# Kernel optimization log

Hardware: AMD Instinct MI355X
Metric: run time of the kernel (lower is better)

Reference implementation:

```python
import jax
jax.config.update("jax_enable_x64", True)
import jax.numpy as jnp
import numpy as np

N_VALUES = 33_554_432   # flattened JaggedTensor values (e.g. 16K batch x 2K multi-hot)
ZCH_SIZE = 4_194_304    # number of managed-collision slots
ID_MAX = 2_147_483_647  # input_hash_size - 1


def setup_inputs() -> dict:
    key = jax.random.key(0)
    k1, k2, k3 = jax.random.split(key, 3)
    values = jax.random.randint(k1, (N_VALUES,), 0, ID_MAX, dtype=jnp.int64)
    mch_sorted_raw_ids = jnp.sort(
        jax.random.randint(k2, (ZCH_SIZE,), 0, ID_MAX, dtype=jnp.int64)
    )
    # remapped ids are a permutation of [0, zch_size)
    mch_remapped_ids_mapping = jax.random.permutation(
        k3, jnp.arange(ZCH_SIZE, dtype=jnp.int64)
    )
    return {
        "values": values,
        "mch_sorted_raw_ids": mch_sorted_raw_ids,
        "mch_remapped_ids_mapping": mch_remapped_ids_mapping,
        "zch_index": ZCH_SIZE,
    }


def reference(values, mch_sorted_raw_ids, mch_remapped_ids_mapping, zch_index):
    # torch.searchsorted default (right=False) == jnp side='left'.
    # Search over table[:-1] so gathered index is always in-bounds (matches torch code).
    searched_indices = jnp.searchsorted(
        mch_sorted_raw_ids[:-1], values, side="left"
    )
    retrieved = mch_sorted_raw_ids[searched_indices]          # gather [N]
    remapped = mch_remapped_ids_mapping[searched_indices]     # gather [N]
    # fused masked-scatter equivalent: hit -> remapped id, miss -> zch sentinel
    return jnp.where(retrieved == values, remapped, jnp.int64(zch_index))
```

## Files before the change

kernel.cpp:

```cpp
#include <hip/hip_runtime.h>


typedef int vint4 __attribute__((ext_vector_type(4)));
typedef unsigned long long u64;

#define HK 2654435761u

__device__ __forceinline__ u64 sig_mask(unsigned v) {
    unsigned h = v * HK;
    return (1ULL << (h >> 26)) | (1ULL << ((h >> 20) & 63)) |
           (1ULL << ((h >> 14) & 63)) | (1ULL << ((h >> 8) & 63));
}

template <int BITS>
__global__ __launch_bounds__(256) void build_aux_scatter(
    const int* __restrict__ table, int m, int* __restrict__ aux) {
    const int SH = 31 - BITS;
    const unsigned NB = 1u << BITS;
    int j = blockIdx.x * blockDim.x + threadIdx.x;
    if (j >= m) return;
    unsigned lo_k = (j == 0) ? 0u : ((((unsigned)table[j - 1]) >> SH) + 1u);
    unsigned hi_k = ((unsigned)table[j]) >> SH;
    for (unsigned k = lo_k; k <= hi_k; ++k) aux[k] = j;
    if (j == m - 1) {
        for (unsigned k = hi_k + 1; k <= NB; ++k) aux[k] = m;
    }
}

template <int BITS>
__global__ __launch_bounds__(256) void build_sigs(
    const int* __restrict__ table, const int* __restrict__ aux, int z,
    u64* __restrict__ filter) {
    const int SH = 31 - BITS;
    const unsigned NB = 1u << BITS;
    unsigned k = blockIdx.x * blockDim.x + threadIdx.x;
    if (k >= NB) return;
    int p = aux[k];
    u64 sig = 0;
    while (p < z && ((((unsigned)table[p]) >> SH) == k)) {
        sig |= sig_mask((unsigned)table[p]);
        ++p;
    }
    filter[k] = sig;
}

template <int BITS>
__device__ __forceinline__ int resolve_window(
    int v, const int* __restrict__ table, const int* __restrict__ mapping,
    const int* __restrict__ aux, int z, int zch) {
    const int SH = 31 - BITS;
    unsigned k = ((unsigned)v) >> SH;
    int lo = aux[k];
    int hi = aux[k + 1];
    int s = lo & ~3;
    int e = (hi + 3) & ~3;
    if (e > z) e = z;
    int cnt = 0;
    bool eq = false;
    for (int p = s; p < e; p += 4) {
        int4 t = *(const int4*)(table + p);
        cnt += (t.x < v) + (t.y < v) + (t.z < v) + (t.w < v);
        eq = eq | (t.x == v) | (t.y == v) | (t.z == v) | (t.w == v);
    }
    if (eq) return mapping[s + cnt];
    return zch;
}

template <int BITS>
__global__ __launch_bounds__(256, 5) void mch_remap_bloom_kernel(
    const vint4* __restrict__ values4,
    const int* __restrict__ table,
    const int* __restrict__ mapping,
    const int* __restrict__ zch_p,
    const int* __restrict__ aux,
    const u64* __restrict__ filter,
    vint4* __restrict__ out4,
    int q4, int z) {
    const int SH = 31 - BITS;

    int zch = *zch_p;
    int i = blockIdx.x * blockDim.x + threadIdx.x;
    if (i >= q4) return;

    vint4 va = __builtin_nontemporal_load(values4 + i);
    vint4 vb = __builtin_nontemporal_load(values4 + i + q4);
    vint4 vc = __builtin_nontemporal_load(values4 + i + 2 * q4);
    vint4 vd = __builtin_nontemporal_load(values4 + i + 3 * q4);
    int v[16] = {va.x, va.y, va.z, va.w, vb.x, vb.y, vb.z, vb.w,
                 vc.x, vc.y, vc.z, vc.w, vd.x, vd.y, vd.z, vd.w};

    u64 w[16];
#pragma unroll
    for (int e = 0; e < 16; ++e) w[e] = filter[((unsigned)v[e]) >> SH];

    unsigned pm = 0;
#pragma unroll
    for (int e = 0; e < 16; ++e) {
        u64 mask = sig_mask((unsigned)v[e]);
        if ((w[e] & mask) == mask) pm |= (1u << e);
    }

    int r[16];
#pragma unroll
    for (int e = 0; e < 16; ++e) r[e] = zch;

    while (pm) {
        int e = __builtin_ctz(pm);
        pm &= pm - 1;
        int a0 = (e & 1) ? v[1]  : v[0];
        int a1 = (e & 1) ? v[3]  : v[2];
        int a2 = (e & 1) ? v[5]  : v[4];
        int a3 = (e & 1) ? v[7]  : v[6];
        int a4 = (e & 1) ? v[9]  : v[8];
        int a5 = (e & 1) ? v[11] : v[10];
        int a6 = (e & 1) ? v[13] : v[12];
        int a7 = (e & 1) ? v[15] : v[14];
        int b0 = (e & 2) ? a1 : a0;
        int b1 = (e & 2) ? a3 : a2;
        int b2 = (e & 2) ? a5 : a4;
        int b3 = (e & 2) ? a7 : a6;
        int c0 = (e & 4) ? b1 : b0;
        int c1 = (e & 4) ? b3 : b2;
        int ve = (e & 8) ? c1 : c0;

        int rr = resolve_window<BITS>(ve, table, mapping, aux, z, zch);

#pragma unroll
        for (int j = 0; j < 16; ++j) r[j] = (e == j) ? rr : r[j];
    }

    vint4 oa, ob, oc, od;
    oa.x = r[0];  oa.y = r[1];  oa.z = r[2];  oa.w = r[3];
    ob.x = r[4];  ob.y = r[5];  ob.z = r[6];  ob.w = r[7];
    oc.x = r[8];  oc.y = r[9];  oc.z = r[10]; oc.w = r[11];
    od.x = r[12]; od.y = r[13]; od.z = r[14]; od.w = r[15];
    __builtin_nontemporal_store(oa, out4 + i);
    __builtin_nontemporal_store(ob, out4 + i + q4);
    __builtin_nontemporal_store(oc, out4 + i + 2 * q4);
    __builtin_nontemporal_store(od, out4 + i + 3 * q4);
}

template <int BITS>
__global__ __launch_bounds__(64) void mch_remap_tail_kernel(
    const int* __restrict__ values, const int* __restrict__ table,
    const int* __restrict__ mapping, const int* __restrict__ zch_p,
    const int* __restrict__ aux, const u64* __restrict__ filter,
    int* __restrict__ out, int start, int n, int z) {
    const int SH = 31 - BITS;
    int i = start + blockIdx.x * blockDim.x + threadIdx.x;
    if (i >= n) return;
    int v = values[i];
    u64 w = filter[((unsigned)v) >> SH];
    u64 mask = sig_mask((unsigned)v);
    int zch = *zch_p;
    out[i] = ((w & mask) == mask)
                 ? resolve_window<BITS>(v, table, mapping, aux, z, zch) : zch;
}

__global__ __launch_bounds__(256) void mch_remap_aux_kernel(
    const int* __restrict__ values, const int* __restrict__ table,
    const int* __restrict__ mapping, const int* __restrict__ zch_p,
    const int* __restrict__ aux, int* __restrict__ out, int n, int z) {
    int zch = *zch_p;
    int i = blockIdx.x * blockDim.x + threadIdx.x;
    if (i >= n) return;
    int v = __builtin_nontemporal_load(values + i);
    out[i] = resolve_window<19>(v, table, mapping, aux, z, zch);
}

template <int BITS>
static void run_bloom(const int* values, const int* table, const int* mapping,
                      const int* zch_p, int* out, int n, int z, int m,
                      void* d_ws, hipStream_t stream) {
    const unsigned NB = 1u << BITS;
    u64* filter = (u64*)d_ws;
    int* aux = (int*)((char*)d_ws + (size_t)NB * 8);
    const int block = 256;

    build_aux_scatter<BITS><<<(m + block - 1) / block, block, 0, stream>>>(
        table, m, aux);
    build_sigs<BITS><<<((int)NB + block - 1) / block, block, 0, stream>>>(
        table, aux, z, filter);

    int q4 = n >> 4;
    if (q4 > 0) {
        mch_remap_bloom_kernel<BITS><<<(q4 + block - 1) / block, block, 0, stream>>>(
            (const vint4*)values, table, mapping, zch_p, aux, filter,
            (vint4*)out, q4, z);
    }
    int done = (q4 << 4);
    if (done < n) {
        mch_remap_tail_kernel<BITS><<<((n - done) + 63) / 64, 64, 0, stream>>>(
            values, table, mapping, zch_p, aux, filter, out, done, n, z);
    }
}

extern "C" void kernel_launch(void* const* d_in, const int* in_sizes, int n_in,
                              void* d_out, int out_size, void* d_ws, size_t ws_size,
                              hipStream_t stream) {
    const int* values  = (const int*)d_in[0];
    const int* table   = (const int*)d_in[1];
    const int* mapping = (const int*)d_in[2];
    const int* zch_p   = (const int*)d_in[3];
    int* out = (int*)d_out;

    int n = in_sizes[0];
    int z = in_sizes[1];
    int m = z - 1;

    const size_t need19 = (size_t)(1u << 19) * 8 + ((size_t)(1u << 19) + 1) * 4;
    const size_t aux19  = ((size_t)(1u << 19) + 1) * 4;
    const int block = 256;

    if (ws_size >= need19) {
        run_bloom<19>(values, table, mapping, zch_p, out, n, z, m, d_ws, stream);
    } else if (ws_size >= aux19) {
        int* aux = (int*)d_ws;
        build_aux_scatter<19><<<(m + block - 1) / block, block, 0, stream>>>(
            table, m, aux);
        mch_remap_aux_kernel<<<(n + block - 1) / block, block, 0, stream>>>(
            values, table, mapping, zch_p, aux, out, n, z);
    }
}
```

Measured before the change: 471.2 us.

## Split bloom remap into two passes partitioned by filter half for cache locality

The main remap kernel now runs twice. Each pass handles only values whose bucket falls in one half of the signature filter, and inactive lanes are redirected to a fixed filter entry so lookups stay within that half. The first pass writes all outputs densely. The second pass writes only hits, with scattered scalar stores. The aim is to keep each half of the filter resident in cache, at the cost of reading the input values twice.

```diff
diff --git a/kernel.cpp b/kernel.cpp
--- a/kernel.cpp
+++ b/kernel.cpp
@@ -66,17 +66,18 @@
     return zch;
 }
 
-template <int BITS>
-__global__ __launch_bounds__(256, 5) void mch_remap_bloom_kernel(
+template <int BITS, int PASS, bool SPARSE>
+__global__ __launch_bounds__(256, 5) void mch_remap_pass_kernel(
     const vint4* __restrict__ values4,
     const int* __restrict__ table,
     const int* __restrict__ mapping,
     const int* __restrict__ zch_p,
     const int* __restrict__ aux,
     const u64* __restrict__ filter,
-    vint4* __restrict__ out4,
+    int* __restrict__ out,
     int q4, int z) {
     const int SH = 31 - BITS;
+    const unsigned PBASE = ((unsigned)PASS) << (BITS - 1);
 
     int zch = *zch_p;
     int i = blockIdx.x * blockDim.x + threadIdx.x;
@@ -89,15 +90,23 @@
     int v[16] = {va.x, va.y, va.z, va.w, vb.x, vb.y, vb.z, vb.w,
                  vc.x, vc.y, vc.z, vc.w, vd.x, vd.y, vd.z, vd.w};
 
+    unsigned act = 0;
     u64 w[16];
 #pragma unroll
-    for (int e = 0; e < 16; ++e) w[e] = filter[((unsigned)v[e]) >> SH];
+    for (int e = 0; e < 16; ++e) {
+        unsigned k = ((unsigned)v[e]) >> SH;
+        bool a = ((k >> (BITS - 1)) == (unsigned)PASS);
+        if (a) act |= (1u << e);
+        unsigned ke = a ? k : PBASE;
+        w[e] = filter[ke];
+    }
+    __builtin_amdgcn_sched_barrier(0);
 
     unsigned pm = 0;
 #pragma unroll
     for (int e = 0; e < 16; ++e) {
         u64 mask = sig_mask((unsigned)v[e]);
-        if ((w[e] & mask) == mask) pm |= (1u << e);
+        if (((w[e] & mask) == mask) && ((act >> e) & 1u)) pm |= (1u << e);
     }
 
     int r[16];
@@ -129,15 +138,23 @@
         for (int j = 0; j < 16; ++j) r[j] = (e == j) ? rr : r[j];
     }
 
-    vint4 oa, ob, oc, od;
-    oa.x = r[0];  oa.y = r[1];  oa.z = r[2];  oa.w = r[3];
-    ob.x = r[4];  ob.y = r[5];  ob.z = r[6];  ob.w = r[7];
-    oc.x = r[8];  oc.y = r[9];  oc.z = r[10]; oc.w = r[11];
-    od.x = r[12]; od.y = r[13]; od.z = r[14]; od.w = r[15];
-    __builtin_nontemporal_store(oa, out4 + i);
-    __builtin_nontemporal_store(ob, out4 + i + q4);
-    __builtin_nontemporal_store(oc, out4 + i + 2 * q4);
-    __builtin_nontemporal_store(od, out4 + i + 3 * q4);
+    if (!SPARSE) {
+        vint4* out4 = (vint4*)out;
+        vint4 oa, ob, oc, od;
+        oa.x = r[0];  oa.y = r[1];  oa.z = r[2];  oa.w = r[3];
+        ob.x = r[4];  ob.y = r[5];  ob.z = r[6];  ob.w = r[7];
+        oc.x = r[8];  oc.y = r[9];  oc.z = r[10]; oc.w = r[11];
+        od.x = r[12]; od.y = r[13]; od.z = r[14]; od.w = r[15];
+        __builtin_nontemporal_store(oa, out4 + i);
+        __builtin_nontemporal_store(ob, out4 + i + q4);
+        __builtin_nontemporal_store(oc, out4 + i + 2 * q4);
+        __builtin_nontemporal_store(od, out4 + i + 3 * q4);
+    } else {
+#pragma unroll
+        for (int e = 0; e < 16; ++e) {
+            if (r[e] != zch) out[4 * (i + (e >> 2) * q4) + (e & 3)] = r[e];
+        }
+    }
 }
 
 template <int BITS>
@@ -184,9 +201,13 @@
 
     int q4 = n >> 4;
     if (q4 > 0) {
-        mch_remap_bloom_kernel<BITS><<<(q4 + block - 1) / block, block, 0, stream>>>(
+        int grid = (q4 + block - 1) / block;
+        mch_remap_pass_kernel<BITS, 0, false><<<grid, block, 0, stream>>>(
             (const vint4*)values, table, mapping, zch_p, aux, filter,
-            (vint4*)out, q4, z);
+            out, q4, z);
+        mch_remap_pass_kernel<BITS, 1, true><<<grid, block, 0, stream>>>(
+            (const vint4*)values, table, mapping, zch_p, aux, filter,
+            out, q4, z);
     }
     int done = (q4 << 4);
     if (done < n) {
```

After: 472.1 us. No clear change (+0.2%).
